# Performance work log

Hardware: AMD Instinct MI355X
Metric: run time of the kernel (lower is better)

Reference implementation:

```python
import jax, jax.numpy as jnp
import numpy as np

NIN, NHID, NDECHID, NOUT = 128, 256, 512, 10
B, N = 32, 4096


def _linear_params(key, fan_in, fan_out):
    kw, kb = jax.random.split(key)
    bound = 1.0 / np.sqrt(fan_in)
    W = jax.random.uniform(kw, (fan_in, fan_out), jnp.float32, -bound, bound)
    b = jax.random.uniform(kb, (fan_out,), jnp.float32, -bound, bound)
    return W, b


def setup_inputs() -> dict:
    key = jax.random.key(0)
    ks = jax.random.split(key, 7)
    x = jax.random.normal(ks[0], (B, N, NIN), jnp.float32)
    W1, b1 = _linear_params(ks[1], NIN, NHID)
    W2, b2 = _linear_params(ks[2], NHID, NHID)
    W3, b3 = _linear_params(ks[3], NHID, NHID)
    D1, c1 = _linear_params(ks[4], NHID, NDECHID)
    D2, c2 = _linear_params(ks[5], NDECHID, NDECHID)
    D3, c3 = _linear_params(ks[6], NDECHID, NOUT)
    return {"x": x, "W1": W1, "b1": b1, "W2": W2, "b2": b2, "W3": W3, "b3": b3,
            "D1": D1, "c1": c1, "D2": D2, "c2": c2, "D3": D3, "c3": c3}


def reference(x, W1, b1, W2, b2, W3, b3, D1, c1, D2, c2, D3, c3):
    # encoder MLP: Linear-ReLU-Linear-ReLU-Linear, then extra ReLU
    h = jax.nn.relu(x @ W1 + b1)            # [B, N, nhid]
    h = jax.nn.relu(h @ W2 + b2)
    h = jax.nn.relu(h @ W3 + b3)            # fused enc output + F.relu
    # mean_{i,j}(h_i * h_j) over the set == (mean_i h)^2 elementwise (exact identity)
    m = jnp.mean(h, axis=1)                  # [B, nhid]
    p = jax.nn.relu(m * m)                   # [B, nhid]
    # decoder MLP
    d = jax.nn.relu(p @ D1 + c1)
    d = jax.nn.relu(d @ D2 + c2)
    return d @ D3 + c3                       # [B, nout]
```

## Files before the change

kernel.cpp:

```cpp
#include <hip/hip_runtime.h>
#include <hip/hip_bf16.h>
#include <stdint.h>


#define NIN   128
#define NHID  256
#define NDEC  512
#define NOUTC 10
#define BATCH 32
#define NTOK  4096
#define MTILE 64
#define NBLK  (BATCH * (NTOK / MTILE))
#define XPAD  136
#define HPAD  264

typedef short bf16x8 __attribute__((ext_vector_type(8)));
typedef float floatx4 __attribute__((ext_vector_type(4)));

__device__ __forceinline__ uint16_t f2b(float f) {
  union { uint32_t u; float f; } v; v.f = f;
  uint32_t r = v.u + 0x7FFFu + ((v.u >> 16) & 1u);
  return (uint16_t)(r >> 16);
}
__device__ __forceinline__ uint32_t pkbf(float lo, float hi) {
  __hip_bfloat162 h = __float22bfloat162_rn(float2{lo, hi});
  union { __hip_bfloat162 h; uint32_t u; } c; c.h = h;
  return c.u;
}

__global__ __launch_bounds__(256) void pack_weights(
    const float* __restrict__ W1, const float* __restrict__ W2,
    const float* __restrict__ W3, uint16_t* __restrict__ pW,
    float* __restrict__ msum) {
  int p = blockIdx.x * blockDim.x + threadIdx.x;
  if (p < BATCH * NHID) msum[p] = 0.f;
  const float* W; int K; int base;
  if (p < 32768)      { W = W1; K = NIN;  base = 0; }
  else if (p < 98304) { W = W2; K = NHID; base = 32768; p -= 32768; }
  else                { W = W3; K = NHID; base = 98304; p -= 98304; }
  int j    = p & 7;
  int ln   = (p >> 3) & 63;
  int rest = p >> 9;
  int KC = K >> 5;
  int kc = rest % KC;
  int mt = rest / KC;
  int m = mt * 16 + (ln & 15);
  int k = kc * 32 + ((ln >> 4) << 3) + j;
  pW[base + (((mt * KC + kc) * 64 + ln) << 3) + j] = f2b(W[k * NHID + m]);
}

__global__ __launch_bounds__(256) void encoder(
    const float* __restrict__ x,
    const uint16_t* __restrict__ pW,
    const float* __restrict__ b1,
    const float* __restrict__ b2,
    const float* __restrict__ b3,
    float* __restrict__ msum) {
  __shared__ __align__(16) uint16_t Hs[MTILE * HPAD];

  const int tid  = threadIdx.x;
  const int wave = tid >> 6;
  const int lane = tid & 63;
  const int l15  = lane & 15;
  const int q    = lane >> 4;
  const int tok0  = blockIdx.x * MTILE;
  const int batch = blockIdx.x >> 6;

  const uint16_t* pW1 = pW;
  const uint16_t* pW2 = pW + 32768;
  const uint16_t* pW3 = pW + 98304;

  {
    const int row = tid >> 2;
    const int c0  = (tid & 3) * 32;
    const float* xr = x + (size_t)(tok0 + row) * NIN + c0;
    for (int i = 0; i < 8; ++i) {
      float4 v = *(const float4*)(xr + i * 4);
      uint2 u = make_uint2(pkbf(v.x, v.y), pkbf(v.z, v.w));
      *(uint2*)&Hs[row * XPAD + c0 + i * 4] = u;
    }
  }
  __syncthreads();

  floatx4 acc[4][4];

  for (int jt = 0; jt < 4; ++jt)
    for (int tt = 0; tt < 4; ++tt)
      acc[jt][tt] = (floatx4){0.f, 0.f, 0.f, 0.f};
#pragma unroll
  for (int kc = 0; kc < 4; ++kc) {
    bf16x8 a[4], b[4];
#pragma unroll
    for (int jt = 0; jt < 4; ++jt)
      a[jt] = *(const bf16x8*)(pW1 + ((((wave * 4 + jt) * 4 + kc) * 64 + lane) << 3));
#pragma unroll
    for (int tt = 0; tt < 4; ++tt)
      b[tt] = *(const bf16x8*)&Hs[(tt * 16 + l15) * XPAD + kc * 32 + q * 8];
#pragma unroll
    for (int jt = 0; jt < 4; ++jt)
#pragma unroll
      for (int tt = 0; tt < 4; ++tt)
        acc[jt][tt] = __builtin_amdgcn_mfma_f32_16x16x32_bf16(
            a[jt], b[tt], acc[jt][tt], 0, 0, 0);
  }
  __syncthreads();

#pragma unroll
  for (int jt = 0; jt < 4; ++jt) {
    const int jbase = wave * 64 + jt * 16 + q * 4;
    const float4 bb = *(const float4*)&b1[jbase];
#pragma unroll
    for (int tt = 0; tt < 4; ++tt) {
      const int t = tt * 16 + l15;
      float v0 = fmaxf(acc[jt][tt][0] + bb.x, 0.f);
      float v1 = fmaxf(acc[jt][tt][1] + bb.y, 0.f);
      float v2 = fmaxf(acc[jt][tt][2] + bb.z, 0.f);
      float v3 = fmaxf(acc[jt][tt][3] + bb.w, 0.f);
      *(uint2*)&Hs[t * HPAD + jbase] = make_uint2(pkbf(v0, v1), pkbf(v2, v3));
    }
  }
  __syncthreads();

  for (int jt = 0; jt < 4; ++jt)
    for (int tt = 0; tt < 4; ++tt)
      acc[jt][tt] = (floatx4){0.f, 0.f, 0.f, 0.f};
#pragma unroll
  for (int kc = 0; kc < 8; ++kc) {
    bf16x8 a[4], b[4];
#pragma unroll
    for (int jt = 0; jt < 4; ++jt)
      a[jt] = *(const bf16x8*)(pW2 + ((((wave * 4 + jt) * 8 + kc) * 64 + lane) << 3));
#pragma unroll
    for (int tt = 0; tt < 4; ++tt)
      b[tt] = *(const bf16x8*)&Hs[(tt * 16 + l15) * HPAD + kc * 32 + q * 8];
#pragma unroll
    for (int jt = 0; jt < 4; ++jt)
#pragma unroll
      for (int tt = 0; tt < 4; ++tt)
        acc[jt][tt] = __builtin_amdgcn_mfma_f32_16x16x32_bf16(
            a[jt], b[tt], acc[jt][tt], 0, 0, 0);
  }
  __syncthreads();
#pragma unroll
  for (int jt = 0; jt < 4; ++jt) {
    const int jbase = wave * 64 + jt * 16 + q * 4;
    const float4 bb = *(const float4*)&b2[jbase];
#pragma unroll
    for (int tt = 0; tt < 4; ++tt) {
      const int t = tt * 16 + l15;
      float v0 = fmaxf(acc[jt][tt][0] + bb.x, 0.f);
      float v1 = fmaxf(acc[jt][tt][1] + bb.y, 0.f);
      float v2 = fmaxf(acc[jt][tt][2] + bb.z, 0.f);
      float v3 = fmaxf(acc[jt][tt][3] + bb.w, 0.f);
      *(uint2*)&Hs[t * HPAD + jbase] = make_uint2(pkbf(v0, v1), pkbf(v2, v3));
    }
  }
  __syncthreads();

  for (int jt = 0; jt < 4; ++jt)
    for (int tt = 0; tt < 4; ++tt)
      acc[jt][tt] = (floatx4){0.f, 0.f, 0.f, 0.f};
#pragma unroll
  for (int kc = 0; kc < 8; ++kc) {
    bf16x8 a[4], b[4];
#pragma unroll
    for (int jt = 0; jt < 4; ++jt)
      a[jt] = *(const bf16x8*)(pW3 + ((((wave * 4 + jt) * 8 + kc) * 64 + lane) << 3));
#pragma unroll
    for (int tt = 0; tt < 4; ++tt)
      b[tt] = *(const bf16x8*)&Hs[(tt * 16 + l15) * HPAD + kc * 32 + q * 8];
#pragma unroll
    for (int jt = 0; jt < 4; ++jt)
#pragma unroll
      for (int tt = 0; tt < 4; ++tt)
        acc[jt][tt] = __builtin_amdgcn_mfma_f32_16x16x32_bf16(
            a[jt], b[tt], acc[jt][tt], 0, 0, 0);
  }
  __syncthreads();

  {
    float4* scratch = (float4*)Hs;
#pragma unroll
    for (int jt = 0; jt < 4; ++jt) {
      const int jbase = wave * 64 + jt * 16 + q * 4;
      const float4 bb = *(const float4*)&b3[jbase];
      float s0 = 0.f, s1 = 0.f, s2 = 0.f, s3 = 0.f;
#pragma unroll
      for (int tt = 0; tt < 4; ++tt) {
        s0 += fmaxf(acc[jt][tt][0] + bb.x, 0.f);
        s1 += fmaxf(acc[jt][tt][1] + bb.y, 0.f);
        s2 += fmaxf(acc[jt][tt][2] + bb.z, 0.f);
        s3 += fmaxf(acc[jt][tt][3] + bb.w, 0.f);
      }
      scratch[((wave * 4 + jt) * 4 + q) * 17 + l15] = (float4){s0, s1, s2, s3};
    }
  }
  __syncthreads();
  {
    const int c = tid >> 2;
    const int r = tid & 3;
    const float* sf = (const float*)Hs;
    float v = 0.f;
#pragma unroll
    for (int l = 0; l < 16; ++l)
      v += sf[c * 68 + l * 4 + r];
    const int wv = c >> 4, jt = (c >> 2) & 3, qq = c & 3;
    const int j = wv * 64 + jt * 16 + qq * 4 + r;
    atomicAdd(&msum[batch * NHID + j], v);
  }
}

__global__ __launch_bounds__(1024) void decoder(
    const float* __restrict__ msum,
    const float* __restrict__ D1, const float* __restrict__ c1,
    const float* __restrict__ D2, const float* __restrict__ c2,
    const float* __restrict__ D3, const float* __restrict__ c3,
    float* __restrict__ out) {
  __shared__ float p[NHID];
  __shared__ float d1[NDEC];
  __shared__ float d2[NDEC];
  __shared__ __align__(16) float red[4096];
  const int b = blockIdx.x, t = threadIdx.x;

  if (t < NHID) {
    float m = msum[b * NHID + t] * (1.f / NTOK);
    p[t] = m * m;
  }
  __syncthreads();

  const int jg = t & 127;
  const int ks = t >> 7;

  {
    const float4* D1v = (const float4*)D1;
    float4 s = {0.f, 0.f, 0.f, 0.f};
    for (int k = ks * 32; k < ks * 32 + 32; ++k) {
      float4 w = D1v[k * 128 + jg];
      float pv = p[k];
      s.x += pv * w.x; s.y += pv * w.y; s.z += pv * w.z; s.w += pv * w.w;
    }
    *(float4*)&red[t * 4] = s;
    __syncthreads();
    if (t < NDEC) {
      float v = c1[t];
#pragma unroll
      for (int i = 0; i < 8; ++i) v += red[i * 512 + t];
      d1[t] = fmaxf(v, 0.f);
    }
    __syncthreads();
  }

  {
    const float4* D2v = (const float4*)D2;
    float4 s = {0.f, 0.f, 0.f, 0.f};
    for (int k = ks * 64; k < ks * 64 + 64; ++k) {
      float4 w = D2v[k * 128 + jg];
      float hv = d1[k];
      s.x += hv * w.x; s.y += hv * w.y; s.z += hv * w.z; s.w += hv * w.w;
    }
    *(float4*)&red[t * 4] = s;
    __syncthreads();
    if (t < NDEC) {
      float v = c2[t];
#pragma unroll
      for (int i = 0; i < 8; ++i) v += red[i * 512 + t];
      d2[t] = fmaxf(v, 0.f);
    }
    __syncthreads();
  }

  {
    const int j3 = t & 15;
    const int kc = t >> 4;
    float s = 0.f;
    if (j3 < NOUTC)
      for (int k = kc * 8; k < kc * 8 + 8; ++k)
        s += d2[k] * D3[k * NOUTC + j3];
    red[t] = s;
    __syncthreads();
    if (t < NOUTC) {
      float v = c3[t];
#pragma unroll
      for (int i = 0; i < 64; ++i) v += red[i * 16 + t];
      out[b * NOUTC + t] = v;
    }
  }
}

extern "C" void kernel_launch(void* const* d_in, const int* in_sizes, int n_in,
                              void* d_out, int out_size, void* d_ws, size_t ws_size,
                              hipStream_t stream) {
  const float* x  = (const float*)d_in[0];
  const float* W1 = (const float*)d_in[1];
  const float* b1 = (const float*)d_in[2];
  const float* W2 = (const float*)d_in[3];
  const float* b2 = (const float*)d_in[4];
  const float* W3 = (const float*)d_in[5];
  const float* b3 = (const float*)d_in[6];
  const float* D1 = (const float*)d_in[7];
  const float* c1 = (const float*)d_in[8];
  const float* D2 = (const float*)d_in[9];
  const float* c2 = (const float*)d_in[10];
  const float* D3 = (const float*)d_in[11];
  const float* c3 = (const float*)d_in[12];

  uint16_t* pW   = (uint16_t*)d_ws;
  float*    msum = (float*)((char*)d_ws + 384 * 1024);

  pack_weights<<<640, 256, 0, stream>>>(W1, W2, W3, pW, msum);
  encoder<<<NBLK, 256, 0, stream>>>(x, pW, b1, b2, b3, msum);
  decoder<<<BATCH, 1024, 0, stream>>>(msum, D1, c1, D2, c2, D3, c3,
                                      (float*)d_out);
}
```

Baseline: 173.2 us.

## Fuse decoder into encoder via last-block-per-batch atomic counter

```diff
diff --git a/kernel.cpp b/kernel.cpp
--- a/kernel.cpp
+++ b/kernel.cpp
@@ -10,7 +10,8 @@
 #define BATCH 32
 #define NTOK  4096
 #define MTILE 64
-#define NBLK  (BATCH * (NTOK / MTILE))
+#define TPB   64
+#define NBLK  (BATCH * TPB)
 #define XPAD  136
 #define HPAD  264
 
@@ -31,9 +32,10 @@
 __global__ __launch_bounds__(256) void pack_weights(
     const float* __restrict__ W1, const float* __restrict__ W2,
     const float* __restrict__ W3, uint16_t* __restrict__ pW,
-    float* __restrict__ msum) {
+    float* __restrict__ msum, int* __restrict__ cnt) {
   int p = blockIdx.x * blockDim.x + threadIdx.x;
   if (p < BATCH * NHID) msum[p] = 0.f;
+  if (p < BATCH) cnt[p] = 0;
   const float* W; int K; int base;
   if (p < 32768)      { W = W1; K = NIN;  base = 0; }
   else if (p < 98304) { W = W2; K = NHID; base = 32768; p -= 32768; }
@@ -55,8 +57,14 @@
     const float* __restrict__ b1,
     const float* __restrict__ b2,
     const float* __restrict__ b3,
-    float* __restrict__ msum) {
+    float* __restrict__ msum,
+    int* __restrict__ cnt,
+    const float* __restrict__ D1, const float* __restrict__ c1,
+    const float* __restrict__ D2, const float* __restrict__ c2,
+    const float* __restrict__ D3, const float* __restrict__ c3,
+    float* __restrict__ out) {
   __shared__ __align__(16) uint16_t Hs[MTILE * HPAD];
+  __shared__ int lastFlag;
 
   const int tid  = threadIdx.x;
   const int wave = tid >> 6;
@@ -208,44 +216,46 @@
     const int j = wv * 64 + jt * 16 + qq * 4 + r;
     atomicAdd(&msum[batch * NHID + j], v);
   }
-}
-
-__global__ __launch_bounds__(1024) void decoder(
-    const float* __restrict__ msum,
-    const float* __restrict__ D1, const float* __restrict__ c1,
-    const float* __restrict__ D2, const float* __restrict__ c2,
-    const float* __restrict__ D3, const float* __restrict__ c3,
-    float* __restrict__ out) {
-  __shared__ float p[NHID];
-  __shared__ float d1[NDEC];
-  __shared__ float d2[NDEC];
-  __shared__ __align__(16) float red[4096];
-  const int b = blockIdx.x, t = threadIdx.x;
-
-  if (t < NHID) {
-    float m = msum[b * NHID + t] * (1.f / NTOK);
-    p[t] = m * m;
-  }
-  __syncthreads();
-
-  const int jg = t & 127;
-  const int ks = t >> 7;
+
+  __syncthreads();
+  if (tid == 0) {
+    __threadfence();
+    int old = atomicAdd(&cnt[batch], 1);
+    lastFlag = (old == TPB - 1);
+  }
+  __syncthreads();
+  if (!lastFlag) return;
+
+  float* F   = (float*)Hs;
+  float* p   = F;
+  float* d1  = F + 256;
+  float* d2  = F + 768;
+  float* red = F + 1280;
+
+  {
+    float m = atomicAdd(&msum[batch * NHID + tid], 0.f) * (1.f / NTOK);
+    p[tid] = m * m;
+  }
+  __syncthreads();
+
+  const int jg = tid & 127;
+  const int ks = tid >> 7;
 
   {
     const float4* D1v = (const float4*)D1;
     float4 s = {0.f, 0.f, 0.f, 0.f};
-    for (int k = ks * 32; k < ks * 32 + 32; ++k) {
+#pragma unroll 4
+    for (int k = ks * 128; k < ks * 128 + 128; ++k) {
       float4 w = D1v[k * 128 + jg];
       float pv = p[k];
       s.x += pv * w.x; s.y += pv * w.y; s.z += pv * w.z; s.w += pv * w.w;
     }
-    *(float4*)&red[t * 4] = s;
-    __syncthreads();
-    if (t < NDEC) {
-      float v = c1[t];
-#pragma unroll
-      for (int i = 0; i < 8; ++i) v += red[i * 512 + t];
-      d1[t] = fmaxf(v, 0.f);
+    *(float4*)&red[tid * 4] = s;
+    __syncthreads();
+#pragma unroll
+    for (int jj = 0; jj < 2; ++jj) {
+      int j = tid + jj * 256;
+      d1[j] = fmaxf(c1[j] + red[j] + red[512 + j], 0.f);
     }
     __syncthreads();
   }
@@ -253,36 +263,36 @@
   {
     const float4* D2v = (const float4*)D2;
     float4 s = {0.f, 0.f, 0.f, 0.f};
-    for (int k = ks * 64; k < ks * 64 + 64; ++k) {
+#pragma unroll 4
+    for (int k = ks * 256; k < ks * 256 + 256; ++k) {
       float4 w = D2v[k * 128 + jg];
       float hv = d1[k];
       s.x += hv * w.x; s.y += hv * w.y; s.z += hv * w.z; s.w += hv * w.w;
     }
-    *(float4*)&red[t * 4] = s;
-    __syncthreads();
-    if (t < NDEC) {
-      float v = c2[t];
-#pragma unroll
-      for (int i = 0; i < 8; ++i) v += red[i * 512 + t];
-      d2[t] = fmaxf(v, 0.f);
-    }
-    __syncthreads();
-  }
-
-  {
-    const int j3 = t & 15;
-    const int kc = t >> 4;
+    *(float4*)&red[tid * 4] = s;
+    __syncthreads();
+#pragma unroll
+    for (int jj = 0; jj < 2; ++jj) {
+      int j = tid + jj * 256;
+      d2[j] = fmaxf(c2[j] + red[j] + red[512 + j], 0.f);
+    }
+    __syncthreads();
+  }
+
+  {
+    const int j3 = tid & 15;
+    const int kc = tid >> 4;
     float s = 0.f;
     if (j3 < NOUTC)
-      for (int k = kc * 8; k < kc * 8 + 8; ++k)
+      for (int k = kc * 32; k < kc * 32 + 32; ++k)
         s += d2[k] * D3[k * NOUTC + j3];
-    red[t] = s;
-    __syncthreads();
-    if (t < NOUTC) {
-      float v = c3[t];
-#pragma unroll
-      for (int i = 0; i < 64; ++i) v += red[i * 16 + t];
-      out[b * NOUTC + t] = v;
+    red[tid] = s;
+    __syncthreads();
+    if (tid < NOUTC) {
+      float v = c3[tid];
+#pragma unroll
+      for (int i = 0; i < 16; ++i) v += red[i * 16 + tid];
+      out[batch * NOUTC + tid] = v;
     }
   }
 }
@@ -306,9 +316,9 @@
 
   uint16_t* pW   = (uint16_t*)d_ws;
   float*    msum = (float*)((char*)d_ws + 384 * 1024);
-
-  pack_weights<<<640, 256, 0, stream>>>(W1, W2, W3, pW, msum);
-  encoder<<<NBLK, 256, 0, stream>>>(x, pW, b1, b2, b3, msum);
-  decoder<<<BATCH, 1024, 0, stream>>>(msum, D1, c1, D2, c2, D3, c3,
-                                      (float*)d_out);
-}
+  int*      cnt  = (int*)((char*)d_ws + 416 * 1024);
+
+  pack_weights<<<640, 256, 0, stream>>>(W1, W2, W3, pW, msum, cnt);
+  encoder<<<NBLK, 256, 0, stream>>>(x, pW, b1, b2, b3, msum, cnt,
+                                    D1, c1, D2, c2, D3, c3, (float*)d_out);
+}
```

New measurement: 231.2 us. 1.33x slower.
